# Performance work log

Hardware: AMD Instinct MI355X
Metric: run time of the kernel (lower is better)

## Reference

```python
import jax, jax.numpy as jnp
import numpy as np

B_IMG = 2
N_PROP = 2000
N_GT = 16
C_FEAT = 256
H_FEAT = 128
W_FEAT = 128
IMG = 1024.0
NUM_CLASSES = 2
BG_THRESH = 0.5          # fg==bg==0.5 -> BETWEEN_THRESHOLDS band is empty
BPI = 512                # batch_size_per_image
NUM_POS_MAX = int(BPI * 0.25)
ENC_W = (1.0, 1.0, 1.0, 1.0, 1.0)
SCALE = 1.0 / 8.0        # feature stride
POOL = 7
SR = 2                   # sampling_ratio
BETA = 1.0 / 9.0
HID = 1024


def _make_boxes(key, shape_prefix, img=IMG):
    kc, ks = jax.random.split(key)
    c = jax.random.uniform(kc, shape_prefix + (2,), minval=0.0, maxval=img)
    s = jax.random.uniform(ks, shape_prefix + (2,), minval=20.0, maxval=200.0)
    lo = jnp.clip(c - 0.5 * s, 0.0, img - 2.0)
    hi = jnp.clip(c + 0.5 * s, lo + 1.0, img)
    return jnp.concatenate([lo, hi], axis=-1)  # [.., x1,y1,x2,y2]


def setup_inputs():
    key = jax.random.key(0)
    ks = jax.random.split(key, 12)
    features = jax.random.normal(ks[0], (B_IMG, C_FEAT, H_FEAT, W_FEAT), dtype=jnp.float32)
    proposals = _make_boxes(ks[1], (B_IMG, N_PROP))
    gt_boxes = _make_boxes(ks[2], (B_IMG, N_GT))
    gt_labels = jax.random.randint(ks[3], (B_IMG, N_GT), 1, NUM_CLASSES, dtype=jnp.int32)
    ka, kb, kt = jax.random.split(ks[4], 3)
    a = jax.random.uniform(ka, (B_IMG, N_GT), minval=10.0, maxval=60.0)
    b = jax.random.uniform(kb, (B_IMG, N_GT), minval=5.0, maxval=30.0)
    th = jax.random.uniform(kt, (B_IMG, N_GT), minval=-np.pi / 2, maxval=np.pi / 2)
    exy = 0.5 * (gt_boxes[..., :2] + gt_boxes[..., 2:])
    gt_ellipses = jnp.stack([a, b, exy[..., 0], exy[..., 1], th], axis=-1)
    d_in = C_FEAT * POOL * POOL
    w1 = jax.random.normal(ks[5], (d_in, HID), dtype=jnp.float32) * 0.02
    b1 = jnp.zeros((HID,), jnp.float32)
    w2 = jax.random.normal(ks[6], (HID, HID), dtype=jnp.float32) * 0.02
    b2 = jnp.zeros((HID,), jnp.float32)
    wc = jax.random.normal(ks[7], (HID, NUM_CLASSES), dtype=jnp.float32) * 0.02
    bc = jnp.zeros((NUM_CLASSES,), jnp.float32)
    wr = jax.random.normal(ks[8], (HID, NUM_CLASSES * 6), dtype=jnp.float32) * 0.02
    br = jnp.zeros((NUM_CLASSES * 6,), jnp.float32)
    return dict(features=features, proposals=proposals, gt_boxes=gt_boxes,
                gt_labels=gt_labels, gt_ellipses=gt_ellipses,
                w1=w1, b1=b1, w2=w2, b2=b2, wc=wc, bc=bc, wr=wr, br=br)


def box_iou(b1, b2):  # [G,4], [P,4] -> [G,P]
    a1 = (b1[:, 2] - b1[:, 0]) * (b1[:, 3] - b1[:, 1])
    a2 = (b2[:, 2] - b2[:, 0]) * (b2[:, 3] - b2[:, 1])
    lt = jnp.maximum(b1[:, None, :2], b2[None, :, :2])
    rb = jnp.minimum(b1[:, None, 2:], b2[None, :, 2:])
    wh = jnp.clip(rb - lt, 0.0)
    inter = wh[..., 0] * wh[..., 1]
    return inter / (a1[:, None] + a2[None, :] - inter)


def encode_ellipses(ell, boxes):  # ell [..,5]=(a,b,cx,cy,theta), boxes [..,4] -> [..,6]
    a, b, ex, ey, th = (ell[..., i] for i in range(5))
    w = jnp.maximum(boxes[..., 2] - boxes[..., 0], 1.0)
    h = jnp.maximum(boxes[..., 3] - boxes[..., 1], 1.0)
    cx = 0.5 * (boxes[..., 0] + boxes[..., 2])
    cy = 0.5 * (boxes[..., 1] + boxes[..., 3])
    wx, wy, wa, wb, wt = ENC_W
    dx = wx * (ex - cx) / w
    dy = wy * (ey - cy) / h
    da = wa * jnp.log(jnp.maximum(2.0 * a, 1e-3) / w)
    db = wb * jnp.log(jnp.maximum(2.0 * b, 1e-3) / h)
    return jnp.stack([dx, dy, da, db, wt * jnp.sin(2.0 * th), wt * jnp.cos(2.0 * th)], axis=-1)


def roi_align(fmap, rois):  # [C,H,W], [R,4] -> [R,C,POOL,POOL]
    C, H, W = fmap.shape
    r = rois * SCALE
    x1, y1, x2, y2 = r[:, 0], r[:, 1], r[:, 2], r[:, 3]
    bw = jnp.maximum(x2 - x1, 1.0) / POOL
    bh = jnp.maximum(y2 - y1, 1.0) / POOL
    S = POOL * SR
    off = (jnp.arange(S, dtype=jnp.float32) + 0.5) / SR  # bin-unit sample offsets
    ys = jnp.clip(y1[:, None] + off[None, :] * bh[:, None], 0.0, H - 1.0)  # [R,S]
    xs = jnp.clip(x1[:, None] + off[None, :] * bw[:, None], 0.0, W - 1.0)
    y0 = jnp.clip(jnp.floor(ys), 0, H - 2).astype(jnp.int32)
    x0 = jnp.clip(jnp.floor(xs), 0, W - 2).astype(jnp.int32)
    ly = ys - y0
    lx = xs - x0
    Ya, Yb = y0[:, :, None], (y0 + 1)[:, :, None]  # [R,S,1]
    Xa, Xb = x0[:, None, :], (x0 + 1)[:, None, :]  # [R,1,S]
    v00 = fmap[:, Ya, Xa]; v01 = fmap[:, Ya, Xb]   # [C,R,S,S]
    v10 = fmap[:, Yb, Xa]; v11 = fmap[:, Yb, Xb]
    wy1 = ly[:, :, None]; wy0 = 1.0 - wy1
    wx1 = lx[:, None, :]; wx0 = 1.0 - wx1
    val = v00 * (wy0 * wx0) + v01 * (wy0 * wx1) + v10 * (wy1 * wx0) + v11 * (wy1 * wx1)
    R = rois.shape[0]
    pooled = val.reshape(C, R, POOL, SR, POOL, SR).mean(axis=(3, 5))
    return pooled.transpose(1, 0, 2, 3)


def reference(features, proposals, gt_boxes, gt_labels, gt_ellipses,
              w1, b1, w2, b2, wc, bc, wr, br):
    B = features.shape[0]
    # add_gt_proposals
    props = jnp.concatenate([proposals, gt_boxes], axis=1)            # [B,P,4]
    # assign_targets_to_proposals: IoU + Matcher (fg=bg=0.5)
    iou = jax.vmap(box_iou)(gt_boxes, props)                          # [B,G,P]
    matched_vals = iou.max(axis=1)
    matches = iou.argmax(axis=1)                                      # [B,P]
    lab = jnp.take_along_axis(gt_labels, matches, axis=1)
    lab = jnp.where(matched_vals < BG_THRESH, 0, lab)                 # background
    # BalancedPositiveNegativeSampler (deterministic, fixed-shape):
    # cap positives at NUM_POS_MAX by random rank, fill rest with random negatives
    rand = jax.random.uniform(jax.random.key(42), lab.shape)
    is_pos = lab > 0
    is_neg = lab == 0
    pos_s = jnp.where(is_pos, rand, -1e9)
    rank = jnp.argsort(jnp.argsort(-pos_s, axis=1), axis=1)
    capped = is_pos & (rank < NUM_POS_MAX)
    prio = jnp.where(capped, rand + 2.0, jnp.where(is_neg, rand, -1e9))
    _, idx = jax.lax.top_k(prio, BPI)                                 # [B,512]
    boxes = jnp.take_along_axis(props, idx[..., None], axis=1)        # [B,512,4]
    labels = jnp.take_along_axis(lab, idx, axis=1)                    # [B,512]
    m = jnp.take_along_axis(matches, idx, axis=1)
    ell = jnp.take_along_axis(gt_ellipses, m[..., None], axis=1)      # [B,512,5]
    targets = encode_ellipses(ell, boxes)                             # [B,512,6]
    # RoIAlign + TwoMLPHead + predictor
    pooled = jax.vmap(roi_align)(features, boxes)                     # [B,512,C,7,7]
    N = B * BPI
    x = pooled.reshape(N, -1)
    x = jax.nn.relu(x @ w1 + b1)
    x = jax.nn.relu(x @ w2 + b2)
    logits = x @ wc + bc                                              # [N,2]
    reg = (x @ wr + br).reshape(N, NUM_CLASSES, 6)
    # ellipse_rcnn_loss
    labels_f = labels.reshape(N)
    t = targets.reshape(N, 6)
    ce = -jnp.take_along_axis(jax.nn.log_softmax(logits, axis=-1), labels_f[:, None], axis=1).mean()
    pred = jnp.take_along_axis(reg, labels_f[:, None, None], axis=1)[:, 0]  # [N,6]
    d = jnp.abs(pred - t)
    sl1 = jnp.where(d < BETA, 0.5 * d * d / BETA, d - 0.5 * BETA)
    reg_loss = jnp.sum(sl1 * (labels_f > 0)[:, None].astype(sl1.dtype)) / N
    return jnp.stack([ce, reg_loss])
```

## Files before the change

### kernel.cpp

```cpp
#include <hip/hip_runtime.h>
#include <hip/hip_bf16.h>
#include <math.h>

#define B_IMG   2
#define N_PROP  2000
#define N_GT    16
#define NPROPS  2016
#define C_FEAT  256
#define H_FEAT  128
#define W_FEAT  128
#define HWF     (H_FEAT*W_FEAT)
#define POOL    7
#define BPI     512
#define NPOSMAX 128
#define NSEL    (B_IMG*BPI)
#define K1      (C_FEAT*POOL*POOL)
#define K1P     12800
#define HID     1024
#define NHEAD   14
#define SPLITK1 8

typedef short bf16x8f __attribute__((ext_vector_type(8)));
typedef float f32x4f  __attribute__((ext_vector_type(4)));
typedef short short4v __attribute__((ext_vector_type(4)));

__device__ __forceinline__ void threefry2x32(unsigned k0, unsigned k1,
                                             unsigned& x0, unsigned& x1) {
  unsigned ks[3] = {k0, k1, k0 ^ k1 ^ 0x1BD11BDAu};
  const int R0[4] = {13, 15, 26, 6};
  const int R1[4] = {17, 29, 16, 24};
  x0 += ks[0]; x1 += ks[1];
#pragma unroll
  for (int g = 0; g < 5; g++) {
    const int* rot = (g & 1) ? R1 : R0;
#pragma unroll
    for (int r = 0; r < 4; r++) {
      x0 += x1;
      x1 = (x1 << rot[r]) | (x1 >> (32 - rot[r]));
      x1 ^= x0;
    }
    x0 += ks[(g + 1) % 3];
    x1 += ks[(g + 2) % 3] + (unsigned)(g + 1);
  }
}

#define PRE_SAMPLE   2
#define PRE_TRANS    (PRE_SAMPLE + 2048)
#define PRE_CAST1    (PRE_TRANS + 3136)
#define PRE_CAST0    (PRE_CAST1 + 256)
#define PRE_TOTAL    (PRE_CAST0 + 512)

__global__ __launch_bounds__(256) void k_pre(const float* __restrict__ proposals,
                                             const float* __restrict__ gt_boxes,
                                             const int* __restrict__ gt_labels,
                                             const float* __restrict__ features,
                                             const float* __restrict__ w1,
                                             const float* __restrict__ w2,
                                             float* __restrict__ prio,
                                             int* __restrict__ plab,
                                             int* __restrict__ matches,
                                             __hip_bfloat16* __restrict__ featT,
                                             __hip_bfloat16* __restrict__ W1T,
                                             __hip_bfloat16* __restrict__ W2T,
                                             __hip_bfloat16* __restrict__ Xb) {
  __shared__ __align__(16) char smem[20800];
  int bid = blockIdx.x;
  int tid = threadIdx.x;
  if (bid < PRE_SAMPLE) {
    float* rs    = (float*)smem;
    float* pos_r = (float*)(smem + 8064);
    short* pos_i = (short*)(smem + 16128);
    float* gtb   = (float*)(smem + 20160);
    int*   gtl   = (int*)(smem + 20416);
    int*   cnt   = (int*)(smem + 20480);
    int b = bid;
    int base = b * NPROPS;
    if (tid == 0) *cnt = 0;
    if (tid < N_GT * 4) gtb[tid] = gt_boxes[b * N_GT * 4 + tid];
    if (tid < N_GT) gtl[tid] = gt_labels[b * N_GT + tid];
    __syncthreads();
    for (int i = tid; i < NPROPS; i += 256) {
      unsigned x0 = 0u, x1 = (unsigned)(base + i);
      threefry2x32(0u, 42u, x0, x1);
      unsigned bits = x0 ^ x1;
      float r = __uint_as_float((bits >> 9) | 0x3F800000u) - 1.0f;
      rs[i] = r;
      float p0, p1, p2, p3;
      if (i < N_PROP) {
        const float4 v = *(const float4*)(proposals + ((size_t)b * N_PROP + i) * 4);
        p0 = v.x; p1 = v.y; p2 = v.z; p3 = v.w;
      } else {
        const float* g = &gtb[(i - N_PROP) * 4];
        p0 = g[0]; p1 = g[1]; p2 = g[2]; p3 = g[3];
      }
      float a2 = (p2 - p0) * (p3 - p1);
      float best = -1.0f; int bg = 0;
#pragma unroll
      for (int g = 0; g < N_GT; g++) {
        float g0 = gtb[g*4], g1 = gtb[g*4+1], g2 = gtb[g*4+2], g3 = gtb[g*4+3];
        float a1 = (g2 - g0) * (g3 - g1);
        float wx = fmaxf(fminf(g2, p2) - fmaxf(g0, p0), 0.0f);
        float wy = fmaxf(fminf(g3, p3) - fmaxf(g1, p1), 0.0f);
        float inter = wx * wy;
        float iou = inter / (a1 + a2 - inter);
        if (iou > best) { best = iou; bg = g; }
      }
      matches[base + i] = bg;
      int lab = (best < 0.5f) ? 0 : gtl[bg];
      plab[base + i] = lab;
      if (lab > 0) {
        int s = atomicAdd(cnt, 1);
        pos_i[s] = (short)i; pos_r[s] = r;
      }
    }
    __syncthreads();
    int P = *cnt;
    for (int s = tid; s < P; s += 256) {
      int i = pos_i[s]; float ri = pos_r[s];
      int ch = 0;
      for (int j = 0; j < P; j++) {
        float rj = pos_r[j]; int ij = pos_i[j];
        ch += (rj > ri || (rj == ri && ij < i)) ? 1 : 0;
      }
      rs[i] = (ch < NPOSMAX) ? (ri + 2.0f) : -1000000000.0f;
    }
    __syncthreads();
    for (int i = tid; i < NPROPS; i += 256) prio[base + i] = rs[i];
  } else if (bid < PRE_TRANS) {
    float (*tile)[65] = (float(*)[65])smem;
    int t = bid - PRE_SAMPLE;
    int b = t >> 10;
    int rem = t & 1023;
    int c0 = (rem >> 8) * 64;
    int s0 = (rem & 255) * 64;
    const float* src = features + (size_t)b * C_FEAT * HWF;
    __hip_bfloat16* dst = featT + (size_t)b * HWF * C_FEAT;
    int hw4 = (tid & 15) * 4, cr = tid >> 4;
#pragma unroll
    for (int p = 0; p < 4; p++) {
      int c = cr + p * 16;
      float4 v = *(const float4*)(src + (size_t)(c0 + c) * HWF + s0 + hw4);
      tile[hw4 + 0][c] = v.x; tile[hw4 + 1][c] = v.y;
      tile[hw4 + 2][c] = v.z; tile[hw4 + 3][c] = v.w;
    }
    __syncthreads();
    int c4 = (tid & 15) * 4, hr = tid >> 4;
#pragma unroll
    for (int p = 0; p < 4; p++) {
      int hw = hr + p * 16;
      __hip_bfloat16 o[4] = {__float2bfloat16(tile[hw][c4]), __float2bfloat16(tile[hw][c4+1]),
                             __float2bfloat16(tile[hw][c4+2]), __float2bfloat16(tile[hw][c4+3])};
      *(short4v*)(dst + (size_t)(s0 + hw) * C_FEAT + c0 + c4) = *(short4v*)o;
    }
  } else if (bid < PRE_CAST1) {
    float (*tile)[65] = (float(*)[65])smem;
    int t = bid - PRE_TRANS;
    int p = t >> 6;
    int rem = t & 63;
    int c0 = (rem & 3) * 64;
    int n0 = (rem >> 2) * 64;
    int n4 = (tid & 15) * 4, ig = tid >> 4;
#pragma unroll
    for (int i = ig; i < 64; i += 16) {
      float4 v = *(const float4*)(w1 + (size_t)((c0 + i) * 49 + p) * HID + n0 + n4);
      tile[i][n4] = v.x; tile[i][n4 + 1] = v.y;
      tile[i][n4 + 2] = v.z; tile[i][n4 + 3] = v.w;
    }
    __syncthreads();
    int c4 = (tid & 15) * 4;
#pragma unroll
    for (int i = ig; i < 64; i += 16) {
      __hip_bfloat16 o[4] = {__float2bfloat16(tile[c4][i]), __float2bfloat16(tile[c4 + 1][i]),
                             __float2bfloat16(tile[c4 + 2][i]), __float2bfloat16(tile[c4 + 3][i])};
      *(short4v*)(W1T + (size_t)(n0 + i) * K1P + p * 256 + c0 + c4) = *(short4v*)o;
    }
  } else if (bid < PRE_CAST0) {
    float (*tile)[65] = (float(*)[65])smem;
    int t = bid - PRE_CAST1;
    int c0 = (t & 15) * 64;
    int n0 = (t >> 4) * 64;
    int n4 = (tid & 15) * 4, ig = tid >> 4;
#pragma unroll
    for (int i = ig; i < 64; i += 16) {
      float4 v = *(const float4*)(w2 + (size_t)(c0 + i) * HID + n0 + n4);
      tile[i][n4] = v.x; tile[i][n4 + 1] = v.y;
      tile[i][n4 + 2] = v.z; tile[i][n4 + 3] = v.w;
    }
    __syncthreads();
    int c4 = (tid & 15) * 4;
#pragma unroll
    for (int i = ig; i < 64; i += 16) {
      __hip_bfloat16 o[4] = {__float2bfloat16(tile[c4][i]), __float2bfloat16(tile[c4 + 1][i]),
                             __float2bfloat16(tile[c4 + 2][i]), __float2bfloat16(tile[c4 + 3][i])};
      *(short4v*)(W2T + (size_t)(n0 + i) * HID + c0 + c4) = *(short4v*)o;
    }
  } else {
    int t = bid - PRE_CAST0;
    __hip_bfloat16* buf = (t >> 8) ? W1T : Xb;
    int tt = (t & 255) * 256 + tid;
    int row = tt >> 6;
    int col4 = (tt & 63) << 2;
    short4v z = {0, 0, 0, 0};
    *(short4v*)(buf + (size_t)row * K1P + K1 + col4) = z;
  }
}

__global__ __launch_bounds__(256) void k_select(const float* __restrict__ prio,
    const float* __restrict__ proposals, const float* __restrict__ gt_boxes,
    const int* __restrict__ matches, const int* __restrict__ plab,
    const float* __restrict__ gt_ell,
    float* __restrict__ sel_boxes, int* __restrict__ sel_labels,
    float* __restrict__ targets) {
  int tid = threadIdx.x;
  int wave = tid >> 6, lane = tid & 63;
  int b = blockIdx.y;
  int base = b * NPROPS;
  int i = blockIdx.x * 4 + wave;
  float pi = prio[base + i];
  int rank = 0;
  for (int j = lane; j < NPROPS; j += 64) {
    float pj = prio[base + j];
    rank += (pj > pi || (pj == pi && j < i)) ? 1 : 0;
  }
#pragma unroll
  for (int off = 32; off > 0; off >>= 1) rank += __shfl_down(rank, off);
  if (lane != 0 || rank >= BPI) return;
  int slot = b * BPI + rank;
  float p0, p1, p2, p3;
  if (i < N_PROP) {
    const float* p = proposals + ((size_t)b * N_PROP + i) * 4;
    p0 = p[0]; p1 = p[1]; p2 = p[2]; p3 = p[3];
  } else {
    const float* p = gt_boxes + ((size_t)b * N_GT + (i - N_PROP)) * 4;
    p0 = p[0]; p1 = p[1]; p2 = p[2]; p3 = p[3];
  }
  sel_boxes[slot * 4 + 0] = p0;
  sel_boxes[slot * 4 + 1] = p1;
  sel_boxes[slot * 4 + 2] = p2;
  sel_boxes[slot * 4 + 3] = p3;
  int lb = plab[base + i];
  sel_labels[slot] = lb;
  int m = matches[base + i];
  const float* e = gt_ell + ((size_t)b * N_GT + m) * 5;
  float ea = e[0], eb = e[1], ex = e[2], ey = e[3], eth = e[4];
  float w = fmaxf(p2 - p0, 1.0f), h = fmaxf(p3 - p1, 1.0f);
  float cx = 0.5f * (p0 + p2), cy = 0.5f * (p1 + p3);
  float* t = targets + (size_t)slot * 6;
  t[0] = (ex - cx) / w;
  t[1] = (ey - cy) / h;
  t[2] = logf(fmaxf(2.0f * ea, 0.001f) / w);
  t[3] = logf(fmaxf(2.0f * eb, 0.001f) / h);
  t[4] = sinf(2.0f * eth);
  t[5] = cosf(2.0f * eth);
}

__global__ __launch_bounds__(256) void k_roialign(const __hip_bfloat16* __restrict__ featT,
                                                  const float* __restrict__ sel_boxes,
                                                  __hip_bfloat16* __restrict__ X) {
  int n = blockIdx.x;
  int py = blockIdx.y;
  int t = threadIdx.x;
  int px = t >> 5;
  int lane32 = t & 31;
  int c = lane32 << 3;
  int b = n >> 9;
  const float* bx = sel_boxes + (size_t)n * 4;
  float x1 = bx[0] * 0.125f, y1 = bx[1] * 0.125f;
  float x2 = bx[2] * 0.125f, y2 = bx[3] * 0.125f;
  float bw = fmaxf(x2 - x1, 1.0f) / 7.0f;
  float bh = fmaxf(y2 - y1, 1.0f) / 7.0f;
  if (px >= 7) return;
  const __hip_bfloat16* base = featT + (size_t)b * HWF * C_FEAT;
  int y0A[2]; float lyA[2];
#pragma unroll
  for (int sy = 0; sy < 2; sy++) {
    float off = ((float)(py * 2 + sy) + 0.5f) * 0.5f;
    float ys = fminf(fmaxf(y1 + off * bh, 0.0f), 127.0f);
    int y0 = (int)fminf(fmaxf(floorf(ys), 0.0f), 126.0f);
    y0A[sy] = y0; lyA[sy] = ys - (float)y0;
  }
  float acc[8] = {};
#pragma unroll
  for (int sx = 0; sx < 2; sx++) {
    float off = ((float)(px * 2 + sx) + 0.5f) * 0.5f;
    float xs = fminf(fmaxf(x1 + off * bw, 0.0f), 127.0f);
    int x0 = (int)fminf(fmaxf(floorf(xs), 0.0f), 126.0f);
    float lx = xs - (float)x0;
#pragma unroll
    for (int sy = 0; sy < 2; sy++) {
      int y0 = y0A[sy]; float ly = lyA[sy];
      const __hip_bfloat16* p = base + ((size_t)(y0 * W_FEAT + x0)) * C_FEAT + c;
      bf16x8f s00 = *(const bf16x8f*)p;
      bf16x8f s01 = *(const bf16x8f*)(p + C_FEAT);
      bf16x8f s10 = *(const bf16x8f*)(p + W_FEAT * C_FEAT);
      bf16x8f s11 = *(const bf16x8f*)(p + W_FEAT * C_FEAT + C_FEAT);
      float w00 = (1.0f - ly) * (1.0f - lx), w01 = (1.0f - ly) * lx;
      float w10 = ly * (1.0f - lx), w11 = ly * lx;
#pragma unroll
      for (int q = 0; q < 8; q++) {
        float v00 = __uint_as_float(((unsigned)(unsigned short)s00[q]) << 16);
        float v01 = __uint_as_float(((unsigned)(unsigned short)s01[q]) << 16);
        float v10 = __uint_as_float(((unsigned)(unsigned short)s10[q]) << 16);
        float v11 = __uint_as_float(((unsigned)(unsigned short)s11[q]) << 16);
        acc[q] += v00 * w00 + v01 * w01 + v10 * w10 + v11 * w11;
      }
    }
  }
  __hip_bfloat16 o[8];
#pragma unroll
  for (int q = 0; q < 8; q++) o[q] = __float2bfloat16(acc[q] * 0.25f);
  *(bf16x8f*)&X[(size_t)n * K1P + (size_t)(py * 7 + px) * C_FEAT + c] = *(bf16x8f*)o;
}

__device__ __forceinline__ void gld_lds16(const __hip_bfloat16* g, __hip_bfloat16* l) {
  __builtin_amdgcn_global_load_lds(
      (const __attribute__((address_space(1))) void*)g,
      (__attribute__((address_space(3))) void*)l, 16, 0, 0);
}

#define G1_KC   1600
#define G1_NKT  25
#define G1_ABUF 16384
#define G1_BUFE 24576

__global__ __launch_bounds__(512, 1) void k_gemm1(const __hip_bfloat16* __restrict__ A,
                                                  const __hip_bfloat16* __restrict__ BT,
                                                  __hip_bfloat16* __restrict__ Pb) {
  __shared__ __align__(16) __hip_bfloat16 lds[3 * G1_BUFE];
  const int lin = blockIdx.x;
  const int pair = (lin & 7) + ((lin >> 6) << 3);
  const int m0 = (pair & 3) * 256;
  const int kz = pair >> 2;
  const int n0 = ((lin >> 3) & 7) * 128;
  const int kbeg = kz * G1_KC;
  const int tid = threadIdx.x;
  const int wave = tid >> 6, lane = tid & 63;
  const int wm = (wave & 3) * 64, wn = (wave >> 2) * 64;
  const int lm = lane & 15, quad = lane >> 4;

  f32x4f acc[4][4] = {};

  auto stage = [&](int kt, int sb) {
    const int kcol = kbeg + kt * 64;
    __hip_bfloat16* lb = lds + sb * G1_BUFE;
#pragma unroll
    for (int u = 0; u < 4; ++u) {
      int idx = tid + u * 512;
      int r = idx >> 3, g = (idx & 7) ^ (r & 7);
      gld_lds16(A + (size_t)(m0 + r) * K1P + kcol + g * 8, lb + idx * 8);
    }
#pragma unroll
    for (int u = 0; u < 2; ++u) {
      int idx = tid + u * 512;
      int r = idx >> 3, g = (idx & 7) ^ (r & 7);
      gld_lds16(BT + (size_t)(n0 + r) * K1P + kcol + g * 8, lb + G1_ABUF + idx * 8);
    }
  };

  stage(0, 0);
  stage(1, 1);
  asm volatile("s_waitcnt vmcnt(6)" ::: "memory");
  __builtin_amdgcn_s_barrier();

  int buf = 0;
  for (int kt = 0; kt < G1_NKT; ++kt) {
    int sb = buf + 2; if (sb >= 3) sb -= 3;
    if (kt + 2 < G1_NKT) stage(kt + 2, sb);
    const __hip_bfloat16* Ab = lds + buf * G1_BUFE;
    const __hip_bfloat16* Bb = Ab + G1_ABUF;
    bf16x8f af[4][2], bf[4][2];
#pragma unroll
    for (int i = 0; i < 4; ++i)
#pragma unroll
      for (int s = 0; s < 2; ++s)
        af[i][s] = *(const bf16x8f*)(Ab + (wm + i * 16 + lm) * 64 +
                                     (((s << 2) + quad) ^ (lm & 7)) * 8);
#pragma unroll
    for (int j = 0; j < 4; ++j)
#pragma unroll
      for (int s = 0; s < 2; ++s)
        bf[j][s] = *(const bf16x8f*)(Bb + (wn + j * 16 + lm) * 64 +
                                     (((s << 2) + quad) ^ (lm & 7)) * 8);
    __builtin_amdgcn_s_setprio(1);
#pragma unroll
    for (int s = 0; s < 2; ++s)
#pragma unroll
      for (int i = 0; i < 4; ++i)
#pragma unroll
        for (int j = 0; j < 4; ++j)
          acc[i][j] = __builtin_amdgcn_mfma_f32_16x16x32_bf16(af[i][s], bf[j][s], acc[i][j], 0, 0, 0);
    __builtin_amdgcn_s_setprio(0);
    if (kt < G1_NKT - 1) {
      if (kt < G1_NKT - 2) asm volatile("s_waitcnt vmcnt(6)" ::: "memory");
      else                 asm volatile("s_waitcnt vmcnt(0)" ::: "memory");
      __builtin_amdgcn_s_barrier();
    }
    buf = (buf == 2) ? 0 : buf + 1;
  }

  int tileoff = ((m0 >> 8) * 8 + (n0 >> 7)) * 32768;
  __hip_bfloat16* dst = Pb + ((size_t)kz << 20) + tileoff + wave * 4096 + lane * 4;
#pragma unroll
  for (int i = 0; i < 4; ++i)
#pragma unroll
    for (int j = 0; j < 4; ++j) {
      __hip_bfloat16 o[4] = {__float2bfloat16(acc[i][j][0]), __float2bfloat16(acc[i][j][1]),
                             __float2bfloat16(acc[i][j][2]), __float2bfloat16(acc[i][j][3])};
      *(short4v*)(dst + (i * 4 + j) * 256) = *(short4v*)o;
    }
}

__global__ __launch_bounds__(256) void k_reduce16(const __hip_bfloat16* __restrict__ Pb,
                                                  const float* __restrict__ bias,
                                                  __hip_bfloat16* __restrict__ O) {
  int m4 = blockIdx.x >> 2;
  int n  = (blockIdx.x & 3) * 256 + threadIdx.x;
  int m0i = m4 >> 6, wavem = (m4 >> 4) & 3, i = (m4 >> 2) & 3, quad = m4 & 3;
  int n0i = n >> 7, wn = (n >> 6) & 1, j = (n >> 4) & 3, lm = n & 15;
  int wave = wavem + wn * 4;
  int elem = (m0i * 8 + n0i) * 32768 + wave * 4096 + (i * 4 + j) * 256 + (quad * 16 + lm) * 4;
  float s0 = 0.0f, s1 = 0.0f, s2 = 0.0f, s3 = 0.0f;
#pragma unroll
  for (int z = 0; z < SPLITK1; z++) {
    short4v v = *(const short4v*)(Pb + ((size_t)z << 20) + elem);
    s0 += __uint_as_float(((unsigned)(unsigned short)v[0]) << 16);
    s1 += __uint_as_float(((unsigned)(unsigned short)v[1]) << 16);
    s2 += __uint_as_float(((unsigned)(unsigned short)v[2]) << 16);
    s3 += __uint_as_float(((unsigned)(unsigned short)v[3]) << 16);
  }
  float bv = bias[n];
  int m = m4 * 4;
  O[(size_t)(m + 0) * HID + n] = __float2bfloat16(fmaxf(s0 + bv, 0.0f));
  O[(size_t)(m + 1) * HID + n] = __float2bfloat16(fmaxf(s1 + bv, 0.0f));
  O[(size_t)(m + 2) * HID + n] = __float2bfloat16(fmaxf(s2 + bv, 0.0f));
  O[(size_t)(m + 3) * HID + n] = __float2bfloat16(fmaxf(s3 + bv, 0.0f));
}

#define G2_NKT  16
#define G2_ABUF 8192
#define G2_BUFE 16384
#define H2P     129

__global__ __launch_bounds__(512, 1) void k_gemm2h(const __hip_bfloat16* __restrict__ A,
                                                   const __hip_bfloat16* __restrict__ BT,
                                                   const float* __restrict__ b2,
                                                   const float* __restrict__ wc,
                                                   const float* __restrict__ wr,
                                                   float* __restrict__ Ypart,
                                                   const float* __restrict__ bc,
                                                   const float* __restrict__ br,
                                                   const int* __restrict__ sel_labels,
                                                   const float* __restrict__ T,
                                                   float* __restrict__ out,
                                                   int* __restrict__ loss_cnt) {
  __shared__ __align__(16) char smem[3 * G2_BUFE * 2];
  __shared__ int lastf;
  __hip_bfloat16* slds = (__hip_bfloat16*)smem;
  float* h2 = (float*)smem;
  float* wh = (float*)(smem + 128 * H2P * 4);
  const int m0 = (blockIdx.x >> 3) * 128;
  const int nb = blockIdx.x & 7;
  const int n0 = nb * 128;
  const int tid = threadIdx.x;
  const int wave = tid >> 6, lane = tid & 63;
  const int wm = (wave & 1) * 64, wn = (wave >> 1) * 32;
  const int lm = lane & 15, quad = lane >> 4;

  f32x4f acc[4][2] = {};

  auto stage = [&](int kt, int sb) {
    const int kcol = kt * 64;
    __hip_bfloat16* lb = slds + sb * G2_BUFE;
#pragma unroll
    for (int u = 0; u < 2; ++u) {
      int idx = tid + u * 512;
      int r = idx >> 3, g = (idx & 7) ^ (r & 7);
      gld_lds16(A + (size_t)(m0 + r) * HID + kcol + g * 8, lb + idx * 8);
    }
#pragma unroll
    for (int u = 0; u < 2; ++u) {
      int idx = tid + u * 512;
      int r = idx >> 3, g = (idx & 7) ^ (r & 7);
      gld_lds16(BT + (size_t)(n0 + r) * HID + kcol + g * 8, lb + G2_ABUF + idx * 8);
    }
  };

  stage(0, 0);
  stage(1, 1);
  asm volatile("s_waitcnt vmcnt(4)" ::: "memory");
  __builtin_amdgcn_s_barrier();

  int buf = 0;
  for (int kt = 0; kt < G2_NKT; ++kt) {
    int sb = buf + 2; if (sb >= 3) sb -= 3;
    if (kt + 2 < G2_NKT) stage(kt + 2, sb);
    const __hip_bfloat16* Ab = slds + buf * G2_BUFE;
    const __hip_bfloat16* Bb = Ab + G2_ABUF;
    bf16x8f af[4][2], bf[2][2];
#pragma unroll
    for (int i = 0; i < 4; ++i)
#pragma unroll
      for (int s = 0; s < 2; ++s)
        af[i][s] = *(const bf16x8f*)(Ab + (wm + i * 16 + lm) * 64 +
                                     (((s << 2) + quad) ^ (lm & 7)) * 8);
#pragma unroll
    for (int j = 0; j < 2; ++j)
#pragma unroll
      for (int s = 0; s < 2; ++s)
        bf[j][s] = *(const bf16x8f*)(Bb + (wn + j * 16 + lm) * 64 +
                                     (((s << 2) + quad) ^ (lm & 7)) * 8);
    __builtin_amdgcn_s_setprio(1);
#pragma unroll
    for (int s = 0; s < 2; ++s)
#pragma unroll
      for (int i = 0; i < 4; ++i)
#pragma unroll
        for (int j = 0; j < 2; ++j)
          acc[i][j] = __builtin_amdgcn_mfma_f32_16x16x32_bf16(af[i][s], bf[j][s], acc[i][j], 0, 0, 0);
    __builtin_amdgcn_s_setprio(0);
    if (kt < G2_NKT - 1) {
      if (kt < G2_NKT - 2) asm volatile("s_waitcnt vmcnt(4)" ::: "memory");
      else                 asm volatile("s_waitcnt vmcnt(0)" ::: "memory");
      __builtin_amdgcn_s_barrier();
    }
    buf = (buf == 2) ? 0 : buf + 1;
  }
  __syncthreads();

  float bb[2];
#pragma unroll
  for (int j = 0; j < 2; ++j) bb[j] = b2[n0 + wn + j * 16 + lm];
#pragma unroll
  for (int i = 0; i < 4; ++i)
#pragma unroll
    for (int j = 0; j < 2; ++j) {
      int col = wn + j * 16 + lm;
#pragma unroll
      for (int r = 0; r < 4; ++r) {
        int row = wm + i * 16 + quad * 4 + r;
        h2[row * H2P + col] = fmaxf(acc[i][j][r] + bb[j], 0.0f);
      }
    }
  for (int idx = tid; idx < 128 * 14; idx += 512) {
    int nl = idx / 14, j = idx - nl * 14;
    wh[idx] = (j < 2) ? wc[(size_t)(n0 + nl) * 2 + j]
                      : wr[(size_t)(n0 + nl) * 12 + (j - 2)];
  }
  __syncthreads();
  {
    int rrow = tid & 127, jg = tid >> 7;
    int j0 = jg * 4, jn = (jg == 3) ? 2 : 4;
    float s[4] = {};
#pragma unroll 4
    for (int k = 0; k < 128; ++k) {
      float h = h2[rrow * H2P + k];
      const float* w = wh + k * 14 + j0;
#pragma unroll
      for (int j = 0; j < 4; ++j) s[j] += h * w[j];
    }
    float* yp = Ypart + ((size_t)nb * NSEL + m0 + rrow) * 16 + j0;
    for (int j = 0; j < jn; ++j) yp[j] = s[j];
  }
  __syncthreads();
  if (tid == 0) {
    __threadfence();
    int old = atomicAdd(loss_cnt, 1);
    lastf = ((old & 63) == 63) ? 1 : 0;
  }
  __syncthreads();
  if (!lastf) return;
  __threadfence();
  float* sc = (float*)smem;
  float* sr = sc + 512;
  float ce_s = 0.0f, rg_s = 0.0f;
#pragma unroll
  for (int half = 0; half < 2; ++half) {
    int n = tid + half * 512;
    float y[14];
#pragma unroll
    for (int j = 0; j < 14; ++j) y[j] = (j < 2) ? bc[j] : br[j - 2];
#pragma unroll
    for (int nb2 = 0; nb2 < 8; ++nb2) {
      const float* p = Ypart + ((size_t)nb2 * NSEL + n) * 16;
      float4 v0 = *(const float4*)(p + 0);
      float4 v1 = *(const float4*)(p + 4);
      float4 v2 = *(const float4*)(p + 8);
      float2 v3 = *(const float2*)(p + 12);
      y[0] += v0.x; y[1] += v0.y; y[2] += v0.z; y[3] += v0.w;
      y[4] += v1.x; y[5] += v1.y; y[6] += v1.z; y[7] += v1.w;
      y[8] += v2.x; y[9] += v2.y; y[10] += v2.z; y[11] += v2.w;
      y[12] += v3.x; y[13] += v3.y;
    }
    int lb = sel_labels[n];
    float mx = fmaxf(y[0], y[1]);
    float lse = mx + logf(expf(y[0] - mx) + expf(y[1] - mx));
    ce_s += lse - (lb ? y[1] : y[0]);
    if (lb > 0) {
      const float beta = 1.0f / 9.0f;
      const float* t = T + (size_t)n * 6;
#pragma unroll
      for (int j = 0; j < 6; j++) {
        float d = fabsf(y[2 + lb * 6 + j] - t[j]);
        rg_s += (d < beta) ? (0.5f * d * d / beta) : (d - 0.5f * beta);
      }
    }
  }
  sc[tid] = ce_s; sr[tid] = rg_s;
  __syncthreads();
  for (int sft = 256; sft > 0; sft >>= 1) {
    if (tid < sft) { sc[tid] += sc[tid + sft]; sr[tid] += sr[tid + sft]; }
    __syncthreads();
  }
  if (tid == 0) {
    out[0] = sc[0] * (1.0f / 1024.0f);
    out[1] = sr[0] * (1.0f / 1024.0f);
  }
}

extern "C" void kernel_launch(void* const* d_in, const int* in_sizes, int n_in,
                              void* d_out, int out_size, void* d_ws, size_t ws_size,
                              hipStream_t stream) {
  const float* features  = (const float*)d_in[0];
  const float* proposals = (const float*)d_in[1];
  const float* gt_boxes  = (const float*)d_in[2];
  const int*   gt_labels = (const int*)d_in[3];
  const float* gt_ell    = (const float*)d_in[4];
  const float* w1 = (const float*)d_in[5];
  const float* b1 = (const float*)d_in[6];
  const float* w2 = (const float*)d_in[7];
  const float* b2 = (const float*)d_in[8];
  const float* wc = (const float*)d_in[9];
  const float* bc = (const float*)d_in[10];
  const float* wr = (const float*)d_in[11];
  const float* br = (const float*)d_in[12];
  float* out = (float*)d_out;

  char* ws = (char*)d_ws;
  size_t off = 0;
  auto take = [&](size_t bytes) -> void* {
    void* p = ws + off;
    off = (off + bytes + 255) & ~(size_t)255;
    return p;
  };
  __hip_bfloat16* Pb = (__hip_bfloat16*)take((size_t)16 * (1 << 20) * 2);
  __hip_bfloat16* featT = Pb;
  __hip_bfloat16* Xb  = (__hip_bfloat16*)take((size_t)NSEL * K1P * 2);
  __hip_bfloat16* W1T = (__hip_bfloat16*)take((size_t)HID * K1P * 2);
  __hip_bfloat16* W2T = (__hip_bfloat16*)take((size_t)HID * HID * 2);
  __hip_bfloat16* H1b = (__hip_bfloat16*)take((size_t)NSEL * HID * 2);
  float* Ypart     = (float*)take((size_t)8 * NSEL * 16 * 4);
  int*   matches   = (int*)take((size_t)B_IMG * NPROPS * 4);
  int*   plab      = (int*)take((size_t)B_IMG * NPROPS * 4);
  float* prio      = (float*)take((size_t)B_IMG * NPROPS * 4);
  float* sel_boxes = (float*)take((size_t)NSEL * 4 * 4);
  int*   sel_lab   = (int*)take((size_t)NSEL * 4);
  float* targets   = (float*)take((size_t)NSEL * 6 * 4);
  int*   loss_cnt  = (int*)take(256);

  k_pre<<<PRE_TOTAL, 256, 0, stream>>>(proposals, gt_boxes, gt_labels, features,
                                       w1, w2, prio, plab, matches,
                                       featT, W1T, W2T, Xb);
  k_select<<<dim3(NPROPS / 4, B_IMG), 256, 0, stream>>>(prio, proposals, gt_boxes,
                                                        matches, plab, gt_ell,
                                                        sel_boxes, sel_lab, targets);
  k_roialign<<<dim3(NSEL, POOL), 256, 0, stream>>>(featT, sel_boxes, Xb);

  k_gemm1<<<256, 512, 0, stream>>>(Xb, W1T, Pb);
  k_reduce16<<<1024, 256, 0, stream>>>(Pb, b1, H1b);
  k_gemm2h<<<64, 512, 0, stream>>>(H1b, W2T, b2, wc, wr, Ypart,
                                   bc, br, sel_lab, targets, out, loss_cnt);
}
```

Measured before the change: 237.3 us.

## Fuse sampling/selection into k_pre and split-K reduction into gemm1 tail

The proposal selection kernel is folded into the sampling blocks of k_pre. It uses an in-shared-memory histogram/bucket rank for negatives, and positives are emitted directly, so the separate k_select launch and its O(N^2) global-memory rank scan go away. The k_reduce16 kernel is also removed: the last split-K block for each output tile, found with an atomic counter, sums the partials and applies bias and ReLU. This saves two launches and a global round-trip, but the two sampling blocks now do more serial work. The tile counter uses (old&7)==7, so it works across calls without being reset, which relies on the counter never being reinitialised to anything else.

```diff
diff --git a/kernel.cpp b/kernel.cpp
--- a/kernel.cpp
+++ b/kernel.cpp
@@ -56,29 +56,64 @@
                                              const float* __restrict__ features,
                                              const float* __restrict__ w1,
                                              const float* __restrict__ w2,
-                                             float* __restrict__ prio,
-                                             int* __restrict__ plab,
-                                             int* __restrict__ matches,
+                                             const float* __restrict__ gt_ell,
                                              __hip_bfloat16* __restrict__ featT,
                                              __hip_bfloat16* __restrict__ W1T,
                                              __hip_bfloat16* __restrict__ W2T,
-                                             __hip_bfloat16* __restrict__ Xb) {
-  __shared__ __align__(16) char smem[20800];
+                                             __hip_bfloat16* __restrict__ Xb,
+                                             float* __restrict__ sel_boxes,
+                                             int* __restrict__ sel_labels,
+                                             float* __restrict__ targets) {
+  __shared__ __align__(16) char smem[29056];
   int bid = blockIdx.x;
   int tid = threadIdx.x;
   if (bid < PRE_SAMPLE) {
     float* rs    = (float*)smem;
+    int*   Hs    = (int*)(smem + 8064);
+    int*   curs  = (int*)(smem + 8064 + 4112);
     float* pos_r = (float*)(smem + 8064);
-    short* pos_i = (short*)(smem + 16128);
-    float* gtb   = (float*)(smem + 20160);
-    int*   gtl   = (int*)(smem + 20416);
-    int*   cnt   = (int*)(smem + 20480);
+    short* glist = (short*)(smem + 16272);
+    short* pos_i = (short*)(smem + 16272);
+    short* mt    = (short*)(smem + 20304);
+    short* lbl   = (short*)(smem + 24336);
+    float* gtb   = (float*)(smem + 28368);
+    float* gte   = (float*)(smem + 28624);
+    int*   gtl   = (int*)(smem + 28944);
+    int*   cnt   = (int*)(smem + 29008);
     int b = bid;
     int base = b * NPROPS;
     if (tid == 0) *cnt = 0;
     if (tid < N_GT * 4) gtb[tid] = gt_boxes[b * N_GT * 4 + tid];
+    if (tid < N_GT * 5) gte[tid] = gt_ell[b * N_GT * 5 + tid];
     if (tid < N_GT) gtl[tid] = gt_labels[b * N_GT + tid];
     __syncthreads();
+
+    auto emitsel = [&](int slot, int i, int lab) {
+      float p0, p1, p2, p3;
+      if (i < N_PROP) {
+        const float4 v = *(const float4*)(proposals + ((size_t)b * N_PROP + i) * 4);
+        p0 = v.x; p1 = v.y; p2 = v.z; p3 = v.w;
+      } else {
+        const float* g = &gtb[(i - N_PROP) * 4];
+        p0 = g[0]; p1 = g[1]; p2 = g[2]; p3 = g[3];
+      }
+      sel_boxes[slot * 4 + 0] = p0;
+      sel_boxes[slot * 4 + 1] = p1;
+      sel_boxes[slot * 4 + 2] = p2;
+      sel_boxes[slot * 4 + 3] = p3;
+      sel_labels[slot] = lab;
+      const float* e = &gte[mt[i] * 5];
+      float w = fmaxf(p2 - p0, 1.0f), h = fmaxf(p3 - p1, 1.0f);
+      float cx = 0.5f * (p0 + p2), cy = 0.5f * (p1 + p3);
+      float* t = targets + (size_t)slot * 6;
+      t[0] = (e[2] - cx) / w;
+      t[1] = (e[3] - cy) / h;
+      t[2] = logf(fmaxf(2.0f * e[0], 0.001f) / w);
+      t[3] = logf(fmaxf(2.0f * e[1], 0.001f) / h);
+      t[4] = sinf(2.0f * e[4]);
+      t[5] = cosf(2.0f * e[4]);
+    };
+
     for (int i = tid; i < NPROPS; i += 256) {
       unsigned x0 = 0u, x1 = (unsigned)(base + i);
       threefry2x32(0u, 42u, x0, x1);
@@ -105,9 +140,9 @@
         float iou = inter / (a1 + a2 - inter);
         if (iou > best) { best = iou; bg = g; }
       }
-      matches[base + i] = bg;
+      mt[i] = (short)bg;
       int lab = (best < 0.5f) ? 0 : gtl[bg];
-      plab[base + i] = lab;
+      lbl[i] = (short)lab;
       if (lab > 0) {
         int s = atomicAdd(cnt, 1);
         pos_i[s] = (short)i; pos_r[s] = r;
@@ -115,6 +150,7 @@
     }
     __syncthreads();
     int P = *cnt;
+    int Pp = (P < NPOSMAX) ? P : NPOSMAX;
     for (int s = tid; s < P; s += 256) {
       int i = pos_i[s]; float ri = pos_r[s];
       int ch = 0;
@@ -122,10 +158,55 @@
         float rj = pos_r[j]; int ij = pos_i[j];
         ch += (rj > ri || (rj == ri && ij < i)) ? 1 : 0;
       }
-      rs[i] = (ch < NPOSMAX) ? (ri + 2.0f) : -1000000000.0f;
-    }
-    __syncthreads();
-    for (int i = tid; i < NPROPS; i += 256) prio[base + i] = rs[i];
+      if (ch < NPOSMAX) emitsel(b * BPI + ch, i, (int)lbl[i]);
+    }
+    __syncthreads();
+    for (int idx = tid; idx < 1025; idx += 256) Hs[idx] = 0;
+    __syncthreads();
+    for (int i = tid; i < NPROPS; i += 256)
+      if (lbl[i] == 0) {
+        int bin = (int)(rs[i] * 1024.0f); if (bin > 1023) bin = 1023;
+        atomicAdd(&Hs[bin], 1);
+      }
+    __syncthreads();
+    for (int off = 1; off < 1024; off <<= 1) {
+      int v[4];
+#pragma unroll
+      for (int k2 = 0; k2 < 4; k2++) {
+        int idx = tid + k2 * 256;
+        v[k2] = Hs[idx] + ((idx + off <= 1024) ? Hs[idx + off] : 0);
+      }
+      __syncthreads();
+#pragma unroll
+      for (int k2 = 0; k2 < 4; k2++) Hs[tid + k2 * 256] = v[k2];
+      __syncthreads();
+    }
+    for (int idx = tid; idx < 1024; idx += 256) curs[idx] = 0;
+    __syncthreads();
+    for (int i = tid; i < NPROPS; i += 256)
+      if (lbl[i] == 0) {
+        int bin = (int)(rs[i] * 1024.0f); if (bin > 1023) bin = 1023;
+        int o = atomicAdd(&curs[bin], 1);
+        glist[Hs[bin + 1] + o] = (short)i;
+      }
+    __syncthreads();
+    for (int i = tid; i < NPROPS; i += 256)
+      if (lbl[i] == 0) {
+        int bin = (int)(rs[i] * 1024.0f); if (bin > 1023) bin = 1023;
+        int bbase = Hs[bin + 1];
+        int cntb = Hs[bin] - bbase;
+        float ri = rs[i];
+        int wr = 0;
+        for (int t = 0; t < cntb; t++) {
+          int j = glist[bbase + t];
+          if (j != i) {
+            float rj = rs[j];
+            wr += (rj > ri || (rj == ri && j < i)) ? 1 : 0;
+          }
+        }
+        int slot = Pp + bbase + wr;
+        if (slot < BPI) emitsel(b * BPI + slot, i, 0);
+      }
   } else if (bid < PRE_TRANS) {
     float (*tile)[65] = (float(*)[65])smem;
     int t = bid - PRE_SAMPLE;
@@ -203,55 +284,6 @@
     short4v z = {0, 0, 0, 0};
     *(short4v*)(buf + (size_t)row * K1P + K1 + col4) = z;
   }
-}
-
-__global__ __launch_bounds__(256) void k_select(const float* __restrict__ prio,
-    const float* __restrict__ proposals, const float* __restrict__ gt_boxes,
-    const int* __restrict__ matches, const int* __restrict__ plab,
-    const float* __restrict__ gt_ell,
-    float* __restrict__ sel_boxes, int* __restrict__ sel_labels,
-    float* __restrict__ targets) {
-  int tid = threadIdx.x;
-  int wave = tid >> 6, lane = tid & 63;
-  int b = blockIdx.y;
-  int base = b * NPROPS;
-  int i = blockIdx.x * 4 + wave;
-  float pi = prio[base + i];
-  int rank = 0;
-  for (int j = lane; j < NPROPS; j += 64) {
-    float pj = prio[base + j];
-    rank += (pj > pi || (pj == pi && j < i)) ? 1 : 0;
-  }
-#pragma unroll
-  for (int off = 32; off > 0; off >>= 1) rank += __shfl_down(rank, off);
-  if (lane != 0 || rank >= BPI) return;
-  int slot = b * BPI + rank;
-  float p0, p1, p2, p3;
-  if (i < N_PROP) {
-    const float* p = proposals + ((size_t)b * N_PROP + i) * 4;
-    p0 = p[0]; p1 = p[1]; p2 = p[2]; p3 = p[3];
-  } else {
-    const float* p = gt_boxes + ((size_t)b * N_GT + (i - N_PROP)) * 4;
-    p0 = p[0]; p1 = p[1]; p2 = p[2]; p3 = p[3];
-  }
-  sel_boxes[slot * 4 + 0] = p0;
-  sel_boxes[slot * 4 + 1] = p1;
-  sel_boxes[slot * 4 + 2] = p2;
-  sel_boxes[slot * 4 + 3] = p3;
-  int lb = plab[base + i];
-  sel_labels[slot] = lb;
-  int m = matches[base + i];
-  const float* e = gt_ell + ((size_t)b * N_GT + m) * 5;
-  float ea = e[0], eb = e[1], ex = e[2], ey = e[3], eth = e[4];
-  float w = fmaxf(p2 - p0, 1.0f), h = fmaxf(p3 - p1, 1.0f);
-  float cx = 0.5f * (p0 + p2), cy = 0.5f * (p1 + p3);
-  float* t = targets + (size_t)slot * 6;
-  t[0] = (ex - cx) / w;
-  t[1] = (ey - cy) / h;
-  t[2] = logf(fmaxf(2.0f * ea, 0.001f) / w);
-  t[3] = logf(fmaxf(2.0f * eb, 0.001f) / h);
-  t[4] = sinf(2.0f * eth);
-  t[5] = cosf(2.0f * eth);
 }
 
 __global__ __launch_bounds__(256) void k_roialign(const __hip_bfloat16* __restrict__ featT,
@@ -325,8 +357,12 @@
 
 __global__ __launch_bounds__(512, 1) void k_gemm1(const __hip_bfloat16* __restrict__ A,
                                                   const __hip_bfloat16* __restrict__ BT,
-                                                  __hip_bfloat16* __restrict__ Pb) {
+                                                  __hip_bfloat16* __restrict__ Pb,
+                                                  const float* __restrict__ b1,
+                                                  __hip_bfloat16* __restrict__ H1b,
+                                                  int* __restrict__ tile_cnt) {
   __shared__ __align__(16) __hip_bfloat16 lds[3 * G1_BUFE];
+  __shared__ int lastf;
   const int lin = blockIdx.x;
   const int pair = (lin & 7) + ((lin >> 6) << 3);
   const int m0 = (pair & 3) * 256;
@@ -398,7 +434,8 @@
     buf = (buf == 2) ? 0 : buf + 1;
   }
 
-  int tileoff = ((m0 >> 8) * 8 + (n0 >> 7)) * 32768;
+  const int tileid = (m0 >> 8) * 8 + (n0 >> 7);
+  const int tileoff = tileid * 32768;
   __hip_bfloat16* dst = Pb + ((size_t)kz << 20) + tileoff + wave * 4096 + lane * 4;
 #pragma unroll
   for (int i = 0; i < 4; ++i)
@@ -408,32 +445,41 @@
                              __float2bfloat16(acc[i][j][2]), __float2bfloat16(acc[i][j][3])};
       *(short4v*)(dst + (i * 4 + j) * 256) = *(short4v*)o;
     }
-}
-
-__global__ __launch_bounds__(256) void k_reduce16(const __hip_bfloat16* __restrict__ Pb,
-                                                  const float* __restrict__ bias,
-                                                  __hip_bfloat16* __restrict__ O) {
-  int m4 = blockIdx.x >> 2;
-  int n  = (blockIdx.x & 3) * 256 + threadIdx.x;
-  int m0i = m4 >> 6, wavem = (m4 >> 4) & 3, i = (m4 >> 2) & 3, quad = m4 & 3;
-  int n0i = n >> 7, wn = (n >> 6) & 1, j = (n >> 4) & 3, lm = n & 15;
-  int wave = wavem + wn * 4;
-  int elem = (m0i * 8 + n0i) * 32768 + wave * 4096 + (i * 4 + j) * 256 + (quad * 16 + lm) * 4;
-  float s0 = 0.0f, s1 = 0.0f, s2 = 0.0f, s3 = 0.0f;
-#pragma unroll
-  for (int z = 0; z < SPLITK1; z++) {
-    short4v v = *(const short4v*)(Pb + ((size_t)z << 20) + elem);
-    s0 += __uint_as_float(((unsigned)(unsigned short)v[0]) << 16);
-    s1 += __uint_as_float(((unsigned)(unsigned short)v[1]) << 16);
-    s2 += __uint_as_float(((unsigned)(unsigned short)v[2]) << 16);
-    s3 += __uint_as_float(((unsigned)(unsigned short)v[3]) << 16);
-  }
-  float bv = bias[n];
-  int m = m4 * 4;
-  O[(size_t)(m + 0) * HID + n] = __float2bfloat16(fmaxf(s0 + bv, 0.0f));
-  O[(size_t)(m + 1) * HID + n] = __float2bfloat16(fmaxf(s1 + bv, 0.0f));
-  O[(size_t)(m + 2) * HID + n] = __float2bfloat16(fmaxf(s2 + bv, 0.0f));
-  O[(size_t)(m + 3) * HID + n] = __float2bfloat16(fmaxf(s3 + bv, 0.0f));
+  __syncthreads();
+  if (tid == 0) {
+    __threadfence();
+    int old = atomicAdd(&tile_cnt[tileid], 1);
+    lastf = ((old & 7) == 7) ? 1 : 0;
+  }
+  __syncthreads();
+  if (!lastf) return;
+  __threadfence();
+#pragma unroll
+  for (int it = 0; it < 16; ++it) {
+    int g = tid + it * 512;
+    int eb = g * 4;
+    int wv = eb >> 12, rem = eb & 4095;
+    int fidx = rem >> 8, lanev = (rem & 255) >> 2;
+    int qd = lanev >> 4, l = lanev & 15;
+    int ii = fidx >> 2, jj = fidx & 3;
+    int mrow = (wv & 3) * 64 + ii * 16 + qd * 4;
+    int ncol = (wv >> 2) * 64 + jj * 16 + l;
+    float s0 = 0.0f, s1 = 0.0f, s2 = 0.0f, s3 = 0.0f;
+#pragma unroll
+    for (int z = 0; z < SPLITK1; z++) {
+      short4v v = *(const short4v*)(Pb + ((size_t)z << 20) + tileoff + eb);
+      s0 += __uint_as_float(((unsigned)(unsigned short)v[0]) << 16);
+      s1 += __uint_as_float(((unsigned)(unsigned short)v[1]) << 16);
+      s2 += __uint_as_float(((unsigned)(unsigned short)v[2]) << 16);
+      s3 += __uint_as_float(((unsigned)(unsigned short)v[3]) << 16);
+    }
+    float bv = b1[n0 + ncol];
+    size_t ob = (size_t)(m0 + mrow) * HID + n0 + ncol;
+    H1b[ob]            = __float2bfloat16(fmaxf(s0 + bv, 0.0f));
+    H1b[ob + HID]      = __float2bfloat16(fmaxf(s1 + bv, 0.0f));
+    H1b[ob + 2 * HID]  = __float2bfloat16(fmaxf(s2 + bv, 0.0f));
+    H1b[ob + 3 * HID]  = __float2bfloat16(fmaxf(s3 + bv, 0.0f));
+  }
 }
 
 #define G2_NKT  16
@@ -649,24 +695,18 @@
   __hip_bfloat16* W2T = (__hip_bfloat16*)take((size_t)HID * HID * 2);
   __hip_bfloat16* H1b = (__hip_bfloat16*)take((size_t)NSEL * HID * 2);
   float* Ypart     = (float*)take((size_t)8 * NSEL * 16 * 4);
-  int*   matches   = (int*)take((size_t)B_IMG * NPROPS * 4);
-  int*   plab      = (int*)take((size_t)B_IMG * NPROPS * 4);
-  float* prio      = (float*)take((size_t)B_IMG * NPROPS * 4);
   float* sel_boxes = (float*)take((size_t)NSEL * 4 * 4);
   int*   sel_lab   = (int*)take((size_t)NSEL * 4);
   float* targets   = (float*)take((size_t)NSEL * 6 * 4);
   int*   loss_cnt  = (int*)take(256);
+  int*   tile_cnt  = (int*)take(256);
 
   k_pre<<<PRE_TOTAL, 256, 0, stream>>>(proposals, gt_boxes, gt_labels, features,
-                                       w1, w2, prio, plab, matches,
-                                       featT, W1T, W2T, Xb);
-  k_select<<<dim3(NPROPS / 4, B_IMG), 256, 0, stream>>>(prio, proposals, gt_boxes,
-                                                        matches, plab, gt_ell,
-                                                        sel_boxes, sel_lab, targets);
+                                       w1, w2, gt_ell, featT, W1T, W2T, Xb,
+                                       sel_boxes, sel_lab, targets);
   k_roialign<<<dim3(NSEL, POOL), 256, 0, stream>>>(featT, sel_boxes, Xb);
 
-  k_gemm1<<<256, 512, 0, stream>>>(Xb, W1T, Pb);
-  k_reduce16<<<1024, 256, 0, stream>>>(Pb, b1, H1b);
+  k_gemm1<<<256, 512, 0, stream>>>(Xb, W1T, Pb, b1, H1b, tile_cnt);
   k_gemm2h<<<64, 512, 0, stream>>>(H1b, W2T, b2, wc, wr, Ypart,
                                    bc, br, sel_lab, targets, out, loss_cnt);
 }
```

Result: slower. 270.3 us (+13.9%).
